# Performance work log

Hardware: AMD Instinct MI355X
Metric: run time of the kernel (lower is better)

Reference implementation:

```python
import jax, jax.numpy as jnp
import numpy as np

NBUS = 33
B33 = [(1,2),(2,3),(3,4),(4,5),(5,6),(6,7),(7,8),(8,9),(9,10),(10,11),(11,12),(12,13),(13,14),(14,15),(15,16),(16,17),(17,18),(2,19),(19,20),(20,21),(21,22),(3,23),(23,24),(24,25),(6,26),(26,27),(27,28),(28,29),(29,30),(30,31),(31,32),(32,33)]


def setup_inputs() -> dict:
    key = jax.random.key(0)
    k1, k2, k3 = jax.random.split(key, 3)
    B, W, M, F = 32, 128, 100, 8
    N, H, GH, K = NBUS, 256, 128, 3
    rng = np.random.default_rng(0)
    br = np.array(B33) - 1
    src = np.concatenate([br[:, 0], br[:, 1]])
    dst = np.concatenate([br[:, 1], br[:, 0]])
    w_half = rng.uniform(0.5, 2.0, size=br.shape[0]).astype(np.float32)
    p = lambda *s: jnp.asarray(rng.normal(0.0, 0.02, size=s).astype(np.float32))
    z = lambda *s: jnp.zeros(s, jnp.float32)
    return {
        'r_seq': jax.random.normal(k1, (B, W, M), jnp.float32),
        'feat_seq': jax.random.normal(k2, (B, W, F), jnp.float32),
        'x_wls_seq': jax.random.normal(k3, (B, W, 2 * N), jnp.float32),
        'edge_index': jnp.asarray(np.stack([src, dst]).astype(np.int32)),
        'edge_weight': jnp.asarray(np.concatenate([w_half, w_half])),
        'pre_w': p(F + 2, GH), 'pre_b': z(GH),
        'tag_w1': p(K + 1, GH, GH), 'tag_b1': z(GH),
        'tag_w2': p(K + 1, GH, GH), 'tag_b2': z(GH),
        'post_w': p(GH, H), 'post_b': z(H),
        'tp_w1': p(M + 2 * N, H), 'tp_b1': z(H),
        'tp_w2': p(H, H), 'tp_b2': z(H),
        'gru_wih0': p(H, 3 * H), 'gru_whh0': p(H, 3 * H), 'gru_bih0': z(3 * H), 'gru_bhh0': z(3 * H),
        'gru_wih1': p(H, 3 * H), 'gru_whh1': p(H, 3 * H), 'gru_bih1': z(3 * H), 'gru_bhh1': z(3 * H),
        'fg_w': p(H, H), 'fg_b': z(H),
        'fs_w': p(H, H), 'fs_b': z(H),
        'gate_w': p(2 * H, H), 'gate_b': z(H),
        'd1_w': p(H, H), 'd1_b': z(H),
        'd2_w': p(H, 2), 'd2_b': z(2),
    }


def _gru_layer(x, wih, whh, bih, bhh):
    # x: (B, W, Din); torch GRU gate order [r, z, n]
    def step(h, xt):
        gi = xt @ wih + bih
        gh = h @ whh + bhh
        ir, iz, inn = jnp.split(gi, 3, axis=-1)
        hr, hz, hn = jnp.split(gh, 3, axis=-1)
        r = jax.nn.sigmoid(ir + hr)
        zt = jax.nn.sigmoid(iz + hz)
        n = jnp.tanh(inn + r * hn)
        h = (1.0 - zt) * n + zt * h
        return h, h
    h0 = jnp.zeros((x.shape[0], whh.shape[0]), x.dtype)
    _, ys = jax.lax.scan(step, h0, jnp.swapaxes(x, 0, 1))
    return jnp.swapaxes(ys, 0, 1)


def _forward(r_seq, feat_seq, x_wls_seq, edge_index, edge_weight,
             pre_w, pre_b, tag_w1, tag_b1, tag_w2, tag_b2, post_w, post_b,
             tp_w1, tp_b1, tp_w2, tp_b2,
             gru_wih0, gru_whh0, gru_bih0, gru_bhh0,
             gru_wih1, gru_whh1, gru_bih1, gru_bhh1,
             fg_w, fg_b, fs_w, fs_b, gate_w, gate_b,
             d1_w, d1_b, d2_w, d2_b):
    B, W, M = r_seq.shape
    N = NBUS
    # ---- spatial branch (batched TAGConv, K=3, 2 layers) ----
    va = x_wls_seq[..., :N, None]
    vm = x_wls_seq[..., N:, None]
    x_nodes = jnp.concatenate([va, vm], axis=-1)                 # (B,W,N,2)
    feat_n = jnp.broadcast_to(feat_seq[:, :, None, :], (B, W, N, feat_seq.shape[-1]))
    gin = jnp.concatenate([feat_n, x_nodes], axis=-1) @ pre_w + pre_b  # (B,W,N,GH)
    g = gin.reshape(B * W, N, gin.shape[-1])
    src, dst = edge_index[0], edge_index[1]
    # gcn_norm (no self-loops), shared across all B*W graph copies
    deg = jnp.zeros((N,), g.dtype).at[dst].add(edge_weight)
    dinv = jnp.where(deg > 0, deg ** -0.5, 0.0)
    norm = dinv[src] * edge_weight * dinv[dst]                   # (E,)

    def prop(h):  # out[i] = sum_{j->i} norm * h[j], batched over graphs
        return jnp.zeros_like(h).at[:, dst].add(h[:, src] * norm[None, :, None])

    def tag(h, Wk, b):  # TAGConv: sum_k A^k h @ W_k + b
        out = h @ Wk[0]
        hk = h
        for k in range(1, Wk.shape[0]):
            hk = prop(hk)
            out = out + hk @ Wk[k]
        return out + b

    g = jax.nn.relu(tag(g, tag_w1, tag_b1))
    g = tag(g, tag_w2, tag_b2)
    g = g.reshape(B, W, N, -1) @ post_w + post_b                 # (B,W,N,H)
    # ---- temporal branch (MLP -> 2-layer GRU); E_time=None skips MHA ----
    s = jnp.concatenate([r_seq, x_wls_seq], axis=-1)
    s = jax.nn.relu(s @ tp_w1 + tp_b1)
    s = jax.nn.relu(s @ tp_w2 + tp_b2)
    s = _gru_layer(s, gru_wih0, gru_whh0, gru_bih0, gru_bhh0)
    s = _gru_layer(s, gru_wih1, gru_whh1, gru_bih1, gru_bhh1)    # (B,W,H)
    # ---- gated fusion + decoder ----
    g_t = g @ fg_w + fg_b                                        # (B,W,N,H)
    s_t = (s @ fs_w + fs_b)[:, :, None, :]                       # (B,W,1,H)
    s_full = jnp.broadcast_to(s_t, g_t.shape)
    alpha = jax.nn.sigmoid(jnp.concatenate([g_t, s_full], axis=-1) @ gate_w + gate_b)
    u = alpha * g_t + (1.0 - alpha) * s_full
    u = jax.nn.relu(u @ d1_w + d1_b) @ d2_w + d2_b               # (B,W,N,2)
    dx = jnp.concatenate([u[..., 0], u[..., 1]], axis=-1)        # (B,W,2N)
    return x_wls_seq + dx


def reference(r_seq, feat_seq, x_wls_seq, edge_index, edge_weight,
              pre_w, pre_b, tag_w1, tag_b1, tag_w2, tag_b2, post_w, post_b,
              tp_w1, tp_b1, tp_w2, tp_b2,
              gru_wih0, gru_whh0, gru_bih0, gru_bhh0,
              gru_wih1, gru_whh1, gru_bih1, gru_bhh1,
              fg_w, fg_b, fs_w, fs_b, gate_w, gate_b,
              d1_w, d1_b, d2_w, d2_b):
    return _forward(r_seq, feat_seq, x_wls_seq, edge_index, edge_weight,
                    pre_w, pre_b, tag_w1, tag_b1, tag_w2, tag_b2, post_w, post_b,
                    tp_w1, tp_b1, tp_w2, tp_b2,
                    gru_wih0, gru_whh0, gru_bih0, gru_bhh0,
                    gru_wih1, gru_whh1, gru_bih1, gru_bhh1,
                    fg_w, fg_b, fs_w, fs_b, gate_w, gate_b,
                    d1_w, d1_b, d2_w, d2_b)
```

## Files before the change

kernel.cpp:

```cpp
#include <hip/hip_runtime.h>
#include <hip/hip_fp16.h>
#include <cmath>

#define DEV __device__ __forceinline__

typedef unsigned short ushortT;
typedef short bs8 __attribute__((ext_vector_type(8)));
typedef float f32x4 __attribute__((ext_vector_type(4)));
typedef _Float16 f16x2 __attribute__((ext_vector_type(2)));

constexpr int kBW = 4096;
constexpr int kM = 100, kF = 8, kN = 33, kH = 256, kGH = 128, kE = 64;

constexpr int OFF_ROWPTR  = 0;
constexpr int OFF_COLSRC  = 64;
constexpr int OFF_COLNORM = 128;
constexpr int OFF_C       = 192;
constexpr int OFF_WC      = 512;
constexpr int OFF_SPRE    = 33280;
constexpr int OFF_GI      = OFF_SPRE + kBW * kH;
constexpr int OFF_SFUSE   = OFF_GI + kBW * 3 * kH;
constexpr int OFF_SGATE   = OFF_SFUSE + kBW * kH;
constexpr int OFF_WQ0     = OFF_SFUSE;
constexpr int OFF_WQ1     = OFF_SFUSE + 98304;
constexpr int WB_TW1  = 0;
constexpr int WB_TW2  = 65536;
constexpr int WB_WC   = 131072;
constexpr int WB_GATE = 163840;
constexpr int WB_D1   = 229376;
constexpr int WB_TOT  = 294912;

DEV float frcp(float x) { return __builtin_amdgcn_rcpf(x); }
DEV float fsig(float x) { return frcp(1.0f + __expf(-x)); }
DEV float ftanh(float x) { float e = __expf(2.0f * x); return 1.0f - 2.0f * frcp(e + 1.0f); }

DEV ushortT f2bf(float x) {
  unsigned u = __float_as_uint(x);
  unsigned r = u + 0x7fffu + ((u >> 16) & 1u);
  return (ushortT)(r >> 16);
}
DEV float bf2f(ushortT u) { return __uint_as_float(((unsigned)u) << 16); }

DEV f32x4 mfma16(bs8 a, bs8 b, f32x4 c) {
  return __builtin_amdgcn_mfma_f32_16x16x32_bf16(a, b, c, 0, 0, 0);
}
DEV bs8 ldb(const ushortT* p) { return *reinterpret_cast<const bs8*>(p); }

#if __has_builtin(__builtin_amdgcn_fdot2)
DEV float dot2(unsigned w, unsigned hp, float acc) {
  f16x2 wv = __builtin_bit_cast(f16x2, w);
  f16x2 hv = __builtin_bit_cast(f16x2, hp);
  return __builtin_amdgcn_fdot2(wv, hv, acc, false);
}
#else
DEV float dot2(unsigned w, unsigned hp, float acc) {
  f16x2 wv = __builtin_bit_cast(f16x2, w);
  f16x2 hv = __builtin_bit_cast(f16x2, hp);
  acc = fmaf((float)wv.x, (float)hv.x, acc);
  acc = fmaf((float)wv.y, (float)hv.y, acc);
  return acc;
}
#endif

__global__ void k_prep(const int* __restrict__ ei, const float* __restrict__ ew,
                       float* __restrict__ ws) {
  if (blockIdx.x != 0 || threadIdx.x != 0) return;
  int* rowptr = (int*)(ws + OFF_ROWPTR);
  int* colsrc = (int*)(ws + OFF_COLSRC);
  float* colnorm = ws + OFF_COLNORM;
  const int* src = ei;
  const int* dst = ei + kE;
  float deg[kN]; int cnt[kN];
  for (int n = 0; n < kN; ++n) { deg[n] = 0.f; cnt[n] = 0; }
  for (int e = 0; e < kE; ++e) { deg[dst[e]] += ew[e]; cnt[dst[e]]++; }
  float dinv[kN];
  for (int n = 0; n < kN; ++n) dinv[n] = deg[n] > 0.f ? 1.0f / sqrtf(deg[n]) : 0.f;
  int pos[kN];
  int run = 0;
  for (int n = 0; n < kN; ++n) { rowptr[n] = run; pos[n] = run; run += cnt[n]; }
  rowptr[kN] = run;
  for (int e = 0; e < kE; ++e) {
    int d = dst[e];
    int p = pos[d]++;
    colsrc[p] = src[e];
    colnorm[p] = dinv[src[e]] * ew[e] * dinv[d];
  }
}

__global__ void k_wcfold(const float* __restrict__ post_w, const float* __restrict__ post_b,
                         const float* __restrict__ fg_w, const float* __restrict__ fg_b,
                         float* __restrict__ ws) {
  const int j = threadIdx.x;
  if ((int)blockIdx.x < kGH) {
    const int k = blockIdx.x;
    float a = 0.f;
    #pragma unroll 4
    for (int m = 0; m < kH; ++m) a = fmaf(post_w[k * kH + m], fg_w[m * kH + j], a);
    ws[OFF_WC + k * kH + j] = a;
  } else {
    float a = fg_b[j];
    #pragma unroll 4
    for (int m = 0; m < kH; ++m) a = fmaf(post_b[m], fg_w[m * kH + j], a);
    ws[OFF_C + j] = a;
  }
}

__global__ void k_wq(const float* __restrict__ w0, const float* __restrict__ w1,
                     float* __restrict__ ws) {
  const int idx = blockIdx.x * 256 + threadIdx.x;
  if (idx >= 2 * 98304) return;
  const int layer = idx / 98304;
  const int rem = idx - layer * 98304;
  const int p = rem / 768, j = rem - p * 768;
  const float* w = layer ? w1 : w0;
  unsigned* dst = (unsigned*)(ws + (layer ? OFF_WQ1 : OFF_WQ0));
  __half2 v = __floats2half2_rn(w[(2 * p) * 768 + j], w[(2 * p + 1) * 768 + j]);
  dst[rem] = *reinterpret_cast<unsigned*>(&v);
}

__global__ void k_wprep(const float* __restrict__ tw1, const float* __restrict__ tw2,
                        const float* __restrict__ gatew, const float* __restrict__ d1w,
                        float* __restrict__ ws) {
  const int idx = blockIdx.x * 256 + threadIdx.x;
  if (idx >= WB_TOT) return;
  ushortT* WB = (ushortT*)(ws + OFF_GI);
  float v; int dst;
  if (idx < 65536) {
    int s = idx >> 14, r = idx & 16383, k = r >> 7, col = r & 127;
    v = tw1[(s << 14) + (k << 7) + col]; dst = WB_TW1 + (s << 14) + (col << 7) + k;
  } else if (idx < 131072) {
    int i = idx - 65536; int s = i >> 14, r = i & 16383, k = r >> 7, col = r & 127;
    v = tw2[(s << 14) + (k << 7) + col]; dst = WB_TW2 + (s << 14) + (col << 7) + k;
  } else if (idx < 163840) {
    int i = idx - 131072; int k = i & 127, col = i >> 7;
    v = ws[OFF_WC + (k << 8) + col]; dst = WB_WC + (col << 7) + k;
  } else if (idx < 229376) {
    int i = idx - 163840; int k = i & 255, col = i >> 8;
    v = gatew[(k << 8) + col]; dst = WB_GATE + (col << 8) + k;
  } else {
    int i = idx - 229376; int k = i & 255, col = i >> 8;
    v = d1w[(k << 8) + col]; dst = WB_D1 + (col << 8) + k;
  }
  WB[dst] = f2bf(v);
}

__global__ __launch_bounds__(256) void k_tpmlp(
    const float* __restrict__ r_seq, const float* __restrict__ x_wls,
    const float* __restrict__ w1, const float* __restrict__ b1,
    const float* __restrict__ w2, const float* __restrict__ b2,
    float* __restrict__ sout) {
  __shared__ float inr[16][kM + 2 * kN];
  __shared__ float h1[16][kH];
  const int bw0 = blockIdx.x * 16, tid = threadIdx.x;
  #pragma unroll
  for (int r = 0; r < 16; ++r) {
    for (int c = tid; c < kM + 2 * kN; c += 256)
      inr[r][c] = (c < kM) ? r_seq[(bw0 + r) * kM + c]
                           : x_wls[(bw0 + r) * 2 * kN + (c - kM)];
  }
  __syncthreads();
  float acc[16];
  {
    const float bb = b1[tid];
    #pragma unroll
    for (int r = 0; r < 16; ++r) acc[r] = bb;
  }
  for (int k = 0; k < kM + 2 * kN; ++k) {
    const float w = w1[k * kH + tid];
    #pragma unroll
    for (int r = 0; r < 16; ++r) acc[r] = fmaf(inr[r][k], w, acc[r]);
  }
  #pragma unroll
  for (int r = 0; r < 16; ++r) h1[r][tid] = fmaxf(acc[r], 0.f);
  __syncthreads();
  {
    const float bb = b2[tid];
    #pragma unroll
    for (int r = 0; r < 16; ++r) acc[r] = bb;
  }
  #pragma unroll 2
  for (int k = 0; k < kH; ++k) {
    const float w = w2[k * kH + tid];
    #pragma unroll
    for (int r = 0; r < 16; ++r) acc[r] = fmaf(h1[r][k], w, acc[r]);
  }
  #pragma unroll
  for (int r = 0; r < 16; ++r) sout[(bw0 + r) * kH + tid] = fmaxf(acc[r], 0.f);
}

__global__ __launch_bounds__(768) void k_gigemm(
    const float* __restrict__ sin, const float* __restrict__ wih,
    const float* __restrict__ bih, float* __restrict__ gi) {
  __shared__ float sr[16][kH];
  const int bw0 = blockIdx.x * 16, tid = threadIdx.x;
  for (int i = tid; i < 16 * kH; i += 768) sr[i >> 8][i & 255] = sin[bw0 * kH + i];
  __syncthreads();
  float acc[16];
  {
    const float bb = bih[tid];
    #pragma unroll
    for (int r = 0; r < 16; ++r) acc[r] = bb;
  }
  #pragma unroll 2
  for (int k = 0; k < kH; ++k) {
    const float w = wih[k * 768 + tid];
    #pragma unroll
    for (int r = 0; r < 16; ++r) acc[r] = fmaf(sr[r][k], w, acc[r]);
  }
  #pragma unroll
  for (int r = 0; r < 16; ++r) gi[(bw0 + r) * 768 + tid] = acc[r];
}

__global__ __launch_bounds__(512, 2) void k_scan(
    const float* __restrict__ gi, const float* __restrict__ wq,
    const float* __restrict__ bhh, float* __restrict__ sout) {
  __shared__ __align__(16) unsigned hpk[2][kH / 2];
  const int b = blockIdx.x, tid = threadIdx.x;
  const int c = tid >> 1, hh = tid & 1;
  const unsigned* wqp = (const unsigned*)wq + hh * 64 * 768 + c;
  unsigned wA[64], wB[64], wC[64];
  #pragma unroll
  for (int p = 0; p < 64; ++p) {
    wA[p] = wqp[p * 768];
    wB[p] = wqp[p * 768 + 256];
    wC[p] = wqp[p * 768 + 512];
  }
  const float bR = bhh[c], bZ = bhh[kH + c], bN = bhh[2 * kH + c];
  if (tid < kH / 2) hpk[0][tid] = 0u;
  float h = 0.f;
  __syncthreads();
  const float* gbase = gi + b * 128 * 768 + c;
  float gA = gbase[0], gB = gbase[256], gC = gbase[512];
  for (int t = 0; t < 128; ++t) {
    const float* gn = gbase + (t < 127 ? (t + 1) : 127) * 768;
    const float nA = gn[0], nB = gn[256], nC = gn[512];
    float aR0 = 0.f, aR1 = 0.f, aZ0 = 0.f, aZ1 = 0.f, aN0 = 0.f, aN1 = 0.f;
    const unsigned* hb = hpk[t & 1] + hh * 64;
    #pragma unroll
    for (int q = 0; q < 16; ++q) {
      const uint4 hp = *reinterpret_cast<const uint4*>(hb + 4 * q);
      aR0 = dot2(wA[4 * q + 0], hp.x, aR0);
      aZ0 = dot2(wB[4 * q + 0], hp.x, aZ0);
      aN0 = dot2(wC[4 * q + 0], hp.x, aN0);
      aR1 = dot2(wA[4 * q + 1], hp.y, aR1);
      aZ1 = dot2(wB[4 * q + 1], hp.y, aZ1);
      aN1 = dot2(wC[4 * q + 1], hp.y, aN1);
      aR0 = dot2(wA[4 * q + 2], hp.z, aR0);
      aZ0 = dot2(wB[4 * q + 2], hp.z, aZ0);
      aN0 = dot2(wC[4 * q + 2], hp.z, aN0);
      aR1 = dot2(wA[4 * q + 3], hp.w, aR1);
      aZ1 = dot2(wB[4 * q + 3], hp.w, aZ1);
      aN1 = dot2(wC[4 * q + 3], hp.w, aN1);
    }
    float aR = aR0 + aR1; aR += __shfl_xor(aR, 1, 64);
    float aZ = aZ0 + aZ1; aZ += __shfl_xor(aZ, 1, 64);
    float aN = aN0 + aN1; aN += __shfl_xor(aN, 1, 64);
    const float r = fsig(gA + bR + aR);
    const float z = fsig(gB + bZ + aZ);
    const float n = ftanh(fmaf(r, aN + bN, gC));
    h = (1.f - z) * n + z * h;
    if (hh == 0) reinterpret_cast<__half*>(hpk[(t + 1) & 1])[c] = __float2half(h);
    else sout[(b * 128 + t) * kH + c] = h;
    gA = nA; gB = nB; gC = nC;
    __syncthreads();
  }
}

__global__ __launch_bounds__(256) void k_fsgate(
    const float* __restrict__ s1, const float* __restrict__ fsw,
    const float* __restrict__ fsb, const float* __restrict__ gw,
    const float* __restrict__ gb, float* __restrict__ sfuse,
    float* __restrict__ sgate) {
  __shared__ float sr[16][kH], sf[16][kH];
  const int bw0 = blockIdx.x * 16, tid = threadIdx.x;
  for (int i = tid; i < 16 * kH; i += 256) sr[i >> 8][i & 255] = s1[bw0 * kH + i];
  __syncthreads();
  float acc[16];
  {
    const float bb = fsb[tid];
    #pragma unroll
    for (int r = 0; r < 16; ++r) acc[r] = bb;
  }
  #pragma unroll 2
  for (int k = 0; k < kH; ++k) {
    const float w = fsw[k * kH + tid];
    #pragma unroll
    for (int r = 0; r < 16; ++r) acc[r] = fmaf(sr[r][k], w, acc[r]);
  }
  #pragma unroll
  for (int r = 0; r < 16; ++r) { sf[r][tid] = acc[r]; sfuse[(bw0 + r) * kH + tid] = acc[r]; }
  __syncthreads();
  {
    const float bb = gb[tid];
    #pragma unroll
    for (int r = 0; r < 16; ++r) acc[r] = bb;
  }
  #pragma unroll 2
  for (int k = 0; k < kH; ++k) {
    const float w = gw[(kH + k) * kH + tid];
    #pragma unroll
    for (int r = 0; r < 16; ++r) acc[r] = fmaf(sf[r][k], w, acc[r]);
  }
  #pragma unroll
  for (int r = 0; r < 16; ++r) sgate[(bw0 + r) * kH + tid] = acc[r];
}


constexpr int BSTR = 136;
constexpr int GSTR = 264;
constexpr int SB0 = 0;
constexpr int SB1 = 36 * BSTR;
constexpr int S_TOT = 2 * 36 * BSTR;

DEV void propb(ushortT* __restrict__ dst, const ushortT* __restrict__ src,
               const int* __restrict__ rp, const int* __restrict__ cs,
               const float* __restrict__ cn) {
  for (int idx = threadIdx.x; idx < kN * 64; idx += 512) {
    const int n = idx >> 6, j2 = idx & 63;
    float a0 = 0.f, a1 = 0.f;
    const int p1 = rp[n + 1];
    for (int p = rp[n]; p < p1; ++p) {
      const unsigned v = *(const unsigned*)(src + cs[p] * BSTR + 2 * j2);
      const float w = cn[p];
      a0 = fmaf(__uint_as_float(v << 16), w, a0);
      a1 = fmaf(__uint_as_float(v & 0xffff0000u), w, a1);
    }
    *(unsigned*)(dst + n * BSTR + 2 * j2) = (unsigned)f2bf(a0) | ((unsigned)f2bf(a1) << 16);
  }
}

template <bool RELU>
DEV void tag_mfma(ushortT* __restrict__ Sb, const ushortT* __restrict__ WT,
                  const float* __restrict__ b, const int* __restrict__ rp,
                  const int* __restrict__ cs, const float* __restrict__ cn,
                  int wv, int lane) {
  const int lr = lane & 15, lg = lane >> 4;
  const int col = wv * 16 + lr;
  f32x4 acc[3];
  #pragma unroll
  for (int i = 0; i < 3; ++i) acc[i] = (f32x4){0.f, 0.f, 0.f, 0.f};
  #pragma unroll
  for (int s = 0; s < 4; ++s) {
    const ushortT* A = Sb + ((s & 1) ? SB1 : SB0);
    ushortT* Bn      = Sb + ((s & 1) ? SB0 : SB1);
    #pragma unroll
    for (int ks = 0; ks < 4; ++ks) {
      const int kof = ks * 32 + lg * 8;
      bs8 a0 = ldb(A + (lr) * BSTR + kof);
      bs8 a1 = ldb(A + (16 + lr) * BSTR + kof);
      bs8 a2 = ldb(A + (32 + lr) * BSTR + kof);
      bs8 bb = ldb(WT + (s << 14) + (col << 7) + kof);
      acc[0] = mfma16(a0, bb, acc[0]);
      acc[1] = mfma16(a1, bb, acc[1]);
      acc[2] = mfma16(a2, bb, acc[2]);
    }
    if (s < 3) {
      propb(Bn, A, rp, cs, cn);
      __syncthreads();
    }
  }
  __syncthreads();
  const float bias = b[col];
  #pragma unroll
  for (int mt = 0; mt < 3; ++mt)
    #pragma unroll
    for (int r = 0; r < 4; ++r) {
      const int row = mt * 16 + lg * 4 + r;
      if (row < kN) {
        float x = acc[mt][r] + bias;
        if (RELU) x = fmaxf(x, 0.f);
        (Sb + SB0)[row * BSTR + col] = f2bf(x);
      }
    }
  __syncthreads();
}

__global__ __launch_bounds__(512, 4) void k_fused(
    const float* __restrict__ feat_seq, const float* __restrict__ x_wls,
    const float* __restrict__ pre_w, const float* __restrict__ pre_b,
    const float* __restrict__ tb1, const float* __restrict__ tb2,
    const float* __restrict__ d1b, const float* __restrict__ d2w,
    const float* __restrict__ d2b, const float* __restrict__ ws,
    const float* __restrict__ sfuse, const float* __restrict__ sgate,
    float* __restrict__ out) {
  __shared__ __align__(16) ushortT S[S_TOT];
  __shared__ float sfrow[kH], sgrow[kH];
  __shared__ float xw[2 * kN];
  __shared__ float featl[kF];
  __shared__ int rp[kN + 1], cs[kE];
  __shared__ float cn[kE];
  __shared__ float part[8][48][2];
  const int tid = threadIdx.x, bw = blockIdx.x;
  const int wv = tid >> 6, lane = tid & 63;
  const int lr = lane & 15, lg = lane >> 4;
  const ushortT* WB = (const ushortT*)(ws + OFF_GI);
  ushortT* GT = S;

  if (tid < kH) sfrow[tid] = sfuse[bw * kH + tid];
  else if (tid < 2 * kH) sgrow[tid - kH] = sgate[bw * kH + (tid - kH)];
  if (tid < 2 * kN) xw[tid] = x_wls[bw * 2 * kN + tid];
  else if (tid >= 66 && tid < 66 + kF) featl[tid - 66] = feat_seq[bw * kF + (tid - 66)];
  if (tid >= 128 && tid < 128 + kN + 1) rp[tid - 128] = ((const int*)(ws + OFF_ROWPTR))[tid - 128];
  if (tid >= 192 && tid < 256) {
    cs[tid - 192] = ((const int*)(ws + OFF_COLSRC))[tid - 192];
    cn[tid - 192] = ws[OFF_COLNORM + (tid - 192)];
  }
  if (tid < 3 * BSTR) {
    S[SB0 + kN * BSTR + tid] = 0;
    S[SB1 + kN * BSTR + tid] = 0;
  }
  __syncthreads();

  for (int idx = tid; idx < kN * kGH; idx += 512) {
    const int n = idx >> 7, j = idx & 127;
    float a = pre_b[j];
    #pragma unroll
    for (int f = 0; f < kF; ++f) a = fmaf(featl[f], pre_w[f * kGH + j], a);
    a = fmaf(xw[n], pre_w[8 * kGH + j], a);
    a = fmaf(xw[kN + n], pre_w[9 * kGH + j], a);
    S[SB0 + n * BSTR + j] = f2bf(a);
  }
  __syncthreads();

  tag_mfma<true >(S, WB + WB_TW1, tb1, rp, cs, cn, wv, lane);
  tag_mfma<false>(S, WB + WB_TW2, tb2, rp, cs, cn, wv, lane);

  {
    f32x4 acc[6];
    #pragma unroll
    for (int i = 0; i < 6; ++i) acc[i] = (f32x4){0.f, 0.f, 0.f, 0.f};
    #pragma unroll
    for (int ks = 0; ks < 4; ++ks) {
      const int kof = ks * 32 + lg * 8;
      bs8 a0 = ldb(S + SB0 + (lr) * BSTR + kof);
      bs8 a1 = ldb(S + SB0 + (16 + lr) * BSTR + kof);
      bs8 a2 = ldb(S + SB0 + (32 + lr) * BSTR + kof);
      #pragma unroll
      for (int nt = 0; nt < 2; ++nt) {
        const int col = (wv * 2 + nt) * 16 + lr;
        bs8 bb = ldb(WB + WB_WC + (col << 7) + kof);
        acc[0 + nt] = mfma16(a0, bb, acc[0 + nt]);
        acc[2 + nt] = mfma16(a1, bb, acc[2 + nt]);
        acc[4 + nt] = mfma16(a2, bb, acc[4 + nt]);
      }
    }
    __syncthreads();
    #pragma unroll
    for (int mt = 0; mt < 3; ++mt)
      #pragma unroll
      for (int nt = 0; nt < 2; ++nt) {
        const int col = (wv * 2 + nt) * 16 + lr;
        const float cb = ws[OFF_C + col];
        const f32x4 v = acc[mt * 2 + nt];
        #pragma unroll
        for (int r = 0; r < 4; ++r) {
          const int row = mt * 16 + lg * 4 + r;
          if (row < kN) GT[row * GSTR + col] = f2bf(v[r] + cb);
        }
      }
    __syncthreads();
  }

  {
    f32x4 acc[6];
    #pragma unroll
    for (int i = 0; i < 6; ++i) acc[i] = (f32x4){0.f, 0.f, 0.f, 0.f};
    #pragma unroll 2
    for (int ks = 0; ks < 8; ++ks) {
      const int kof = ks * 32 + lg * 8;
      const int r2 = (32 + lr) < 36 ? (32 + lr) : 35;
      bs8 a0 = ldb(GT + (lr) * GSTR + kof);
      bs8 a1 = ldb(GT + (16 + lr) * GSTR + kof);
      bs8 a2 = ldb(GT + r2 * GSTR + kof);
      #pragma unroll
      for (int nt = 0; nt < 2; ++nt) {
        const int col = (wv * 2 + nt) * 16 + lr;
        bs8 bb = ldb(WB + WB_GATE + (col << 8) + kof);
        acc[0 + nt] = mfma16(a0, bb, acc[0 + nt]);
        acc[2 + nt] = mfma16(a1, bb, acc[2 + nt]);
        acc[4 + nt] = mfma16(a2, bb, acc[4 + nt]);
      }
    }
    #pragma unroll
    for (int mt = 0; mt < 3; ++mt)
      #pragma unroll
      for (int nt = 0; nt < 2; ++nt) {
        const int col = (wv * 2 + nt) * 16 + lr;
        const float sg = sgrow[col], sf = sfrow[col];
        #pragma unroll
        for (int r = 0; r < 4; ++r) {
          const int row = mt * 16 + lg * 4 + r;
          if (row < kN) {
            const float al = fsig(acc[mt * 2 + nt][r] + sg);
            const float gt = bf2f(GT[row * GSTR + col]);
            acc[mt * 2 + nt][r] = al * gt + (1.f - al) * sf;
          }
        }
      }
    __syncthreads();
    #pragma unroll
    for (int mt = 0; mt < 3; ++mt)
      #pragma unroll
      for (int nt = 0; nt < 2; ++nt) {
        const int col = (wv * 2 + nt) * 16 + lr;
        #pragma unroll
        for (int r = 0; r < 4; ++r) {
          const int row = mt * 16 + lg * 4 + r;
          if (row < kN) GT[row * GSTR + col] = f2bf(acc[mt * 2 + nt][r]);
        }
      }
    __syncthreads();
  }

  {
    f32x4 acc[6];
    #pragma unroll
    for (int i = 0; i < 6; ++i) acc[i] = (f32x4){0.f, 0.f, 0.f, 0.f};
    #pragma unroll 2
    for (int ks = 0; ks < 8; ++ks) {
      const int kof = ks * 32 + lg * 8;
      const int r2 = (32 + lr) < 36 ? (32 + lr) : 35;
      bs8 a0 = ldb(GT + (lr) * GSTR + kof);
      bs8 a1 = ldb(GT + (16 + lr) * GSTR + kof);
      bs8 a2 = ldb(GT + r2 * GSTR + kof);
      #pragma unroll
      for (int nt = 0; nt < 2; ++nt) {
        const int col = (wv * 2 + nt) * 16 + lr;
        bs8 bb = ldb(WB + WB_D1 + (col << 8) + kof);
        acc[0 + nt] = mfma16(a0, bb, acc[0 + nt]);
        acc[2 + nt] = mfma16(a1, bb, acc[2 + nt]);
        acc[4 + nt] = mfma16(a2, bb, acc[4 + nt]);
      }
    }
    float p0[3][4], p1[3][4];
    #pragma unroll
    for (int mt = 0; mt < 3; ++mt)
      #pragma unroll
      for (int r = 0; r < 4; ++r) { p0[mt][r] = 0.f; p1[mt][r] = 0.f; }
    #pragma unroll
    for (int nt = 0; nt < 2; ++nt) {
      const int col = (wv * 2 + nt) * 16 + lr;
      const float db = d1b[col];
      const float2 dp = *reinterpret_cast<const float2*>(d2w + col * 2);
      #pragma unroll
      for (int mt = 0; mt < 3; ++mt)
        #pragma unroll
        for (int r = 0; r < 4; ++r) {
          const float v = fmaxf(acc[mt * 2 + nt][r] + db, 0.f);
          p0[mt][r] = fmaf(v, dp.x, p0[mt][r]);
          p1[mt][r] = fmaf(v, dp.y, p1[mt][r]);
        }
    }
    #pragma unroll
    for (int mt = 0; mt < 3; ++mt)
      #pragma unroll
      for (int r = 0; r < 4; ++r) {
        #pragma unroll
        for (int off = 1; off < 16; off <<= 1) {
          p0[mt][r] += __shfl_xor(p0[mt][r], off, 64);
          p1[mt][r] += __shfl_xor(p1[mt][r], off, 64);
        }
      }
    if (lr == 0) {
      #pragma unroll
      for (int mt = 0; mt < 3; ++mt)
        #pragma unroll
        for (int r = 0; r < 4; ++r) {
          const int row = mt * 16 + lg * 4 + r;
          part[wv][row][0] = p0[mt][r];
          part[wv][row][1] = p1[mt][r];
        }
    }
    __syncthreads();
    if (tid < 66) {
      const int c = tid >= 33 ? 1 : 0;
      const int n = tid - 33 * c;
      float s = d2b[c];
      #pragma unroll
      for (int w = 0; w < 8; ++w) s += part[w][n][c];
      out[bw * 66 + tid] = xw[tid] + s;
    }
  }
}

extern "C" void kernel_launch(void* const* d_in, const int* in_sizes, int n_in,
                              void* d_out, int out_size, void* d_ws, size_t ws_size,
                              hipStream_t stream) {
  const float* r_seq  = (const float*)d_in[0];
  const float* feat   = (const float*)d_in[1];
  const float* x_wls  = (const float*)d_in[2];
  const int*   eidx   = (const int*)d_in[3];
  const float* ew     = (const float*)d_in[4];
  const float* pre_w  = (const float*)d_in[5];
  const float* pre_b  = (const float*)d_in[6];
  const float* tag_w1 = (const float*)d_in[7];
  const float* tag_b1 = (const float*)d_in[8];
  const float* tag_w2 = (const float*)d_in[9];
  const float* tag_b2 = (const float*)d_in[10];
  const float* post_w = (const float*)d_in[11];
  const float* post_b = (const float*)d_in[12];
  const float* tp_w1  = (const float*)d_in[13];
  const float* tp_b1  = (const float*)d_in[14];
  const float* tp_w2  = (const float*)d_in[15];
  const float* tp_b2  = (const float*)d_in[16];
  const float* wih0   = (const float*)d_in[17];
  const float* whh0   = (const float*)d_in[18];
  const float* bih0   = (const float*)d_in[19];
  const float* bhh0   = (const float*)d_in[20];
  const float* wih1   = (const float*)d_in[21];
  const float* whh1   = (const float*)d_in[22];
  const float* bih1   = (const float*)d_in[23];
  const float* bhh1   = (const float*)d_in[24];
  const float* fg_w   = (const float*)d_in[25];
  const float* fg_b   = (const float*)d_in[26];
  const float* fs_w   = (const float*)d_in[27];
  const float* fs_b   = (const float*)d_in[28];
  const float* gate_w = (const float*)d_in[29];
  const float* gate_b = (const float*)d_in[30];
  const float* d1_w   = (const float*)d_in[31];
  const float* d1_b   = (const float*)d_in[32];
  const float* d2_w   = (const float*)d_in[33];
  const float* d2_b   = (const float*)d_in[34];
  float* ws = (float*)d_ws;
  float* outp = (float*)d_out;

  k_prep<<<1, 64, 0, stream>>>(eidx, ew, ws);
  k_wcfold<<<kGH + 1, kH, 0, stream>>>(post_w, post_b, fg_w, fg_b, ws);
  k_wq<<<768, 256, 0, stream>>>(whh0, whh1, ws);
  k_tpmlp<<<kBW / 16, 256, 0, stream>>>(r_seq, x_wls, tp_w1, tp_b1, tp_w2, tp_b2,
                                        ws + OFF_SPRE);
  k_gigemm<<<kBW / 16, 768, 0, stream>>>(ws + OFF_SPRE, wih0, bih0, ws + OFF_GI);
  k_scan<<<32, 512, 0, stream>>>(ws + OFF_GI, ws + OFF_WQ0, bhh0, ws + OFF_SPRE);
  k_gigemm<<<kBW / 16, 768, 0, stream>>>(ws + OFF_SPRE, wih1, bih1, ws + OFF_GI);
  k_scan<<<32, 512, 0, stream>>>(ws + OFF_GI, ws + OFF_WQ1, bhh1, ws + OFF_SPRE);
  k_wprep<<<(WB_TOT + 255) / 256, 256, 0, stream>>>(tag_w1, tag_w2, gate_w, d1_w, ws);
  k_fsgate<<<kBW / 16, 256, 0, stream>>>(ws + OFF_SPRE, fs_w, fs_b, gate_w, gate_b,
                                         ws + OFF_SFUSE, ws + OFF_SGATE);
  k_fused<<<kBW, 512, 0, stream>>>(feat, x_wls, pre_w, pre_b, tag_b1, tag_b2,
                                   d1_b, d2_w, d2_b, ws, ws + OFF_SFUSE,
                                   ws + OFF_SGATE, outp);
}
```

Baseline: 967.1 us.

## Batch GRU recurrence over 16 sequences per block using bf16 MFMA

The recurrent GRU scan previously ran one sequence per block and did the hidden-to-hidden matvec with fp16 packed dot products, using 32 blocks. It now packs 16 sequences into each block's shared hidden-state tile and computes the recurrent GEMM with bf16 16x16x32 MFMA, with weights held in registers as MFMA B fragments. Only 2 blocks are launched. The weight-quantization kernel is changed to emit transposed bf16 weights. The aim is to cut the per-step latency of the serial recurrence. In exchange the hidden state is stored in bf16, which has less mantissa than fp16, and the per-step gate-input loads are scattered and not prefetched.

```diff
diff --git a/kernel.cpp b/kernel.cpp
--- a/kernel.cpp
+++ b/kernel.cpp
@@ -45,22 +45,6 @@
   return __builtin_amdgcn_mfma_f32_16x16x32_bf16(a, b, c, 0, 0, 0);
 }
 DEV bs8 ldb(const ushortT* p) { return *reinterpret_cast<const bs8*>(p); }
-
-#if __has_builtin(__builtin_amdgcn_fdot2)
-DEV float dot2(unsigned w, unsigned hp, float acc) {
-  f16x2 wv = __builtin_bit_cast(f16x2, w);
-  f16x2 hv = __builtin_bit_cast(f16x2, hp);
-  return __builtin_amdgcn_fdot2(wv, hv, acc, false);
-}
-#else
-DEV float dot2(unsigned w, unsigned hp, float acc) {
-  f16x2 wv = __builtin_bit_cast(f16x2, w);
-  f16x2 hv = __builtin_bit_cast(f16x2, hp);
-  acc = fmaf((float)wv.x, (float)hv.x, acc);
-  acc = fmaf((float)wv.y, (float)hv.y, acc);
-  return acc;
-}
-#endif
 
 __global__ void k_prep(const int* __restrict__ ei, const float* __restrict__ ew,
                        float* __restrict__ ws) {
@@ -108,14 +92,13 @@
 __global__ void k_wq(const float* __restrict__ w0, const float* __restrict__ w1,
                      float* __restrict__ ws) {
   const int idx = blockIdx.x * 256 + threadIdx.x;
-  if (idx >= 2 * 98304) return;
-  const int layer = idx / 98304;
-  const int rem = idx - layer * 98304;
-  const int p = rem / 768, j = rem - p * 768;
+  if (idx >= 2 * 196608) return;
+  const int layer = idx / 196608;
+  const int rem = idx - layer * 196608;
+  const int col = rem >> 8, k = rem & 255;
   const float* w = layer ? w1 : w0;
-  unsigned* dst = (unsigned*)(ws + (layer ? OFF_WQ1 : OFF_WQ0));
-  __half2 v = __floats2half2_rn(w[(2 * p) * 768 + j], w[(2 * p + 1) * 768 + j]);
-  dst[rem] = *reinterpret_cast<unsigned*>(&v);
+  ushortT* dst = (ushortT*)(ws + (layer ? OFF_WQ1 : OFF_WQ0));
+  dst[rem] = f2bf(w[k * 768 + col]);
 }
 
 __global__ void k_wprep(const float* __restrict__ tw1, const float* __restrict__ tw2,
@@ -214,55 +197,81 @@
 __global__ __launch_bounds__(512, 2) void k_scan(
     const float* __restrict__ gi, const float* __restrict__ wq,
     const float* __restrict__ bhh, float* __restrict__ sout) {
-  __shared__ __align__(16) unsigned hpk[2][kH / 2];
-  const int b = blockIdx.x, tid = threadIdx.x;
-  const int c = tid >> 1, hh = tid & 1;
-  const unsigned* wqp = (const unsigned*)wq + hh * 64 * 768 + c;
-  unsigned wA[64], wB[64], wC[64];
-  #pragma unroll
-  for (int p = 0; p < 64; ++p) {
-    wA[p] = wqp[p * 768];
-    wB[p] = wqp[p * 768 + 256];
-    wC[p] = wqp[p * 768 + 512];
-  }
-  const float bR = bhh[c], bZ = bhh[kH + c], bN = bhh[2 * kH + c];
-  if (tid < kH / 2) hpk[0][tid] = 0u;
-  float h = 0.f;
-  __syncthreads();
-  const float* gbase = gi + b * 128 * 768 + c;
-  float gA = gbase[0], gB = gbase[256], gC = gbase[512];
+  __shared__ __align__(16) ushortT ha[2][16 * 264];
+  const int tid = threadIdx.x;
+  const int wv = tid >> 6, lane = tid & 63;
+  const int lr = lane & 15, lg = lane >> 4;
+  const int blk16 = blockIdx.x * 16;
+  const ushortT* wq2 = (const ushortT*)wq;
+  bs8 wB[2][3][8];
+  #pragma unroll
+  for (int cg = 0; cg < 2; ++cg) {
+    const int col = wv * 32 + cg * 16 + lr;
+    #pragma unroll
+    for (int g = 0; g < 3; ++g)
+      #pragma unroll
+      for (int ks = 0; ks < 8; ++ks)
+        wB[cg][g][ks] = ldb(wq2 + ((g * 256 + col) << 8) + ks * 32 + lg * 8);
+  }
+  float bR[2], bZ[2], bN[2];
+  #pragma unroll
+  for (int cg = 0; cg < 2; ++cg) {
+    const int col = wv * 32 + cg * 16 + lr;
+    bR[cg] = bhh[col]; bZ[cg] = bhh[256 + col]; bN[cg] = bhh[512 + col];
+  }
+  float ho[2][4];
+  #pragma unroll
+  for (int cg = 0; cg < 2; ++cg)
+    #pragma unroll
+    for (int r = 0; r < 4; ++r) ho[cg][r] = 0.f;
+  for (int i = tid; i < 16 * 264; i += 512) ha[0][i] = 0;
+  __syncthreads();
+  int cur = 0;
   for (int t = 0; t < 128; ++t) {
-    const float* gn = gbase + (t < 127 ? (t + 1) : 127) * 768;
-    const float nA = gn[0], nB = gn[256], nC = gn[512];
-    float aR0 = 0.f, aR1 = 0.f, aZ0 = 0.f, aZ1 = 0.f, aN0 = 0.f, aN1 = 0.f;
-    const unsigned* hb = hpk[t & 1] + hh * 64;
-    #pragma unroll
-    for (int q = 0; q < 16; ++q) {
-      const uint4 hp = *reinterpret_cast<const uint4*>(hb + 4 * q);
-      aR0 = dot2(wA[4 * q + 0], hp.x, aR0);
-      aZ0 = dot2(wB[4 * q + 0], hp.x, aZ0);
-      aN0 = dot2(wC[4 * q + 0], hp.x, aN0);
-      aR1 = dot2(wA[4 * q + 1], hp.y, aR1);
-      aZ1 = dot2(wB[4 * q + 1], hp.y, aZ1);
-      aN1 = dot2(wC[4 * q + 1], hp.y, aN1);
-      aR0 = dot2(wA[4 * q + 2], hp.z, aR0);
-      aZ0 = dot2(wB[4 * q + 2], hp.z, aZ0);
-      aN0 = dot2(wC[4 * q + 2], hp.z, aN0);
-      aR1 = dot2(wA[4 * q + 3], hp.w, aR1);
-      aZ1 = dot2(wB[4 * q + 3], hp.w, aZ1);
-      aN1 = dot2(wC[4 * q + 3], hp.w, aN1);
-    }
-    float aR = aR0 + aR1; aR += __shfl_xor(aR, 1, 64);
-    float aZ = aZ0 + aZ1; aZ += __shfl_xor(aZ, 1, 64);
-    float aN = aN0 + aN1; aN += __shfl_xor(aN, 1, 64);
-    const float r = fsig(gA + bR + aR);
-    const float z = fsig(gB + bZ + aZ);
-    const float n = ftanh(fmaf(r, aN + bN, gC));
-    h = (1.f - z) * n + z * h;
-    if (hh == 0) reinterpret_cast<__half*>(hpk[(t + 1) & 1])[c] = __float2half(h);
-    else sout[(b * 128 + t) * kH + c] = h;
-    gA = nA; gB = nB; gC = nC;
+    float giv[2][3][4];
+    #pragma unroll
+    for (int cg = 0; cg < 2; ++cg) {
+      const int col = wv * 32 + cg * 16 + lr;
+      #pragma unroll
+      for (int g = 0; g < 3; ++g)
+        #pragma unroll
+        for (int r = 0; r < 4; ++r)
+          giv[cg][g][r] =
+              gi[((blk16 + lg * 4 + r) * 128 + t) * 768 + g * 256 + col];
+    }
+    f32x4 acc[2][3];
+    #pragma unroll
+    for (int cg = 0; cg < 2; ++cg)
+      #pragma unroll
+      for (int g = 0; g < 3; ++g) acc[cg][g] = (f32x4){0.f, 0.f, 0.f, 0.f};
+    const ushortT* A = ha[cur];
+    #pragma unroll
+    for (int ks = 0; ks < 8; ++ks) {
+      bs8 a = ldb(A + lr * 264 + ks * 32 + lg * 8);
+      #pragma unroll
+      for (int cg = 0; cg < 2; ++cg)
+        #pragma unroll
+        for (int g = 0; g < 3; ++g)
+          acc[cg][g] = mfma16(a, wB[cg][g][ks], acc[cg][g]);
+    }
+    ushortT* Hn = ha[cur ^ 1];
+    #pragma unroll
+    for (int cg = 0; cg < 2; ++cg) {
+      const int col = wv * 32 + cg * 16 + lr;
+      #pragma unroll
+      for (int r = 0; r < 4; ++r) {
+        const int bt = lg * 4 + r;
+        const float R = fsig(giv[cg][0][r] + bR[cg] + acc[cg][0][r]);
+        const float Z = fsig(giv[cg][1][r] + bZ[cg] + acc[cg][1][r]);
+        const float Nv = ftanh(fmaf(R, acc[cg][2][r] + bN[cg], giv[cg][2][r]));
+        const float hn = (1.f - Z) * Nv + Z * ho[cg][r];
+        ho[cg][r] = hn;
+        Hn[bt * 264 + col] = f2bf(hn);
+        sout[((blk16 + bt) * 128 + t) * 256 + col] = hn;
+      }
+    }
     __syncthreads();
+    cur ^= 1;
   }
 }
 
@@ -626,13 +635,13 @@
 
   k_prep<<<1, 64, 0, stream>>>(eidx, ew, ws);
   k_wcfold<<<kGH + 1, kH, 0, stream>>>(post_w, post_b, fg_w, fg_b, ws);
-  k_wq<<<768, 256, 0, stream>>>(whh0, whh1, ws);
+  k_wq<<<1536, 256, 0, stream>>>(whh0, whh1, ws);
   k_tpmlp<<<kBW / 16, 256, 0, stream>>>(r_seq, x_wls, tp_w1, tp_b1, tp_w2, tp_b2,
                                         ws + OFF_SPRE);
   k_gigemm<<<kBW / 16, 768, 0, stream>>>(ws + OFF_SPRE, wih0, bih0, ws + OFF_GI);
-  k_scan<<<32, 512, 0, stream>>>(ws + OFF_GI, ws + OFF_WQ0, bhh0, ws + OFF_SPRE);
+  k_scan<<<2, 512, 0, stream>>>(ws + OFF_GI, ws + OFF_WQ0, bhh0, ws + OFF_SPRE);
   k_gigemm<<<kBW / 16, 768, 0, stream>>>(ws + OFF_SPRE, wih1, bih1, ws + OFF_GI);
-  k_scan<<<32, 512, 0, stream>>>(ws + OFF_GI, ws + OFF_WQ1, bhh1, ws + OFF_SPRE);
+  k_scan<<<2, 512, 0, stream>>>(ws + OFF_GI, ws + OFF_WQ1, bhh1, ws + OFF_SPRE);
   k_wprep<<<(WB_TOT + 255) / 256, 256, 0, stream>>>(tag_w1, tag_w2, gate_w, d1_w, ws);
   k_fsgate<<<kBW / 16, 256, 0, stream>>>(ws + OFF_SPRE, fs_w, fs_b, gate_w, gate_b,
                                          ws + OFF_SFUSE, ws + OFF_SGATE);
```

New measurement: 1.539 ms. 59.2% more time.
